# Kernel optimization log

Hardware: AMD Instinct MI355X
Metric: run time of the kernel (lower is better)

Reference implementation:

```python
import jax, jax.numpy as jnp
import numpy as np

K = 31            # kernel_size
P = K // 2        # padding
EPS = 1e-05
STRENGTH = 1.0


def _box_filter(x):
    """31x31 mean box filter with zero padding, done as two separable 1D passes.
    Exactly equals F.conv2d(x, ones(K,K)/K^2, padding=P) since the box kernel
    is separable and padding is zero-fill."""
    kh = jnp.ones((1, 1, K, 1), x.dtype) / K  # vertical pass
    kw = jnp.ones((1, 1, 1, K), x.dtype) / K  # horizontal pass
    dn = jax.lax.conv_dimension_numbers(x.shape, kh.shape, ('NCHW', 'OIHW', 'NCHW'))
    x = jax.lax.conv_general_dilated(x, kh, (1, 1), [(P, P), (0, 0)], dimension_numbers=dn)
    x = jax.lax.conv_general_dilated(x, kw, (1, 1), [(0, 0), (P, P)], dimension_numbers=dn)
    return x


def setup_inputs() -> dict:
    key = jax.random.key(0)
    # (B, 1, H, W) image in [0, 1]
    x = jax.random.uniform(key, (32, 1, 1024, 1024), dtype=jnp.float32)
    return {"x": x}


def reference(x):
    local_mean = _box_filter(x)
    local_sq_mean = _box_filter(x * x)
    local_var = local_sq_mean - local_mean * local_mean
    local_std = jnp.sqrt(jnp.maximum(local_var, EPS))  # clamp(min=eps) then sqrt
    normalized = (x - local_mean) / (local_std + EPS)
    enhanced = jax.nn.sigmoid(normalized * 0.5)
    return x * (1.0 - STRENGTH) + enhanced * STRENGTH
```

## Files before the change

### kernel.cpp

```cpp
#include <hip/hip_runtime.h>
#include <math.h>


#define KSZ   31
#define PAD   15
#define IMG_H 1024
#define IMG_W 1024
#define SH    32
#define RPP   4
#define PHASES (SH / RPP)
#define NT    256
#define LROW  66
#define LBUF  (16 * LROW)
#define EPSV  1e-5f

__global__ __launch_bounds__(NT, 4)
void lcn_fused_kernel(const float* __restrict__ x, float* __restrict__ out) {
    const int cpx = gridDim.x >> 3;
    const int bid = (blockIdx.x & 7) * cpx + (blockIdx.x >> 3);

    const int t     = threadIdx.x;
    const int chunk = bid & 31;
    const int b     = bid >> 5;
    const int y0    = chunk * SH;

    const float* img  = x   + (size_t)b * (IMG_H * IMG_W);
    float*       oimg = out + (size_t)b * (IMG_H * IMG_W);

    __shared__ float2 vbuf[RPP][LBUF];

    for (int i = t; i < RPP * LBUF; i += NT)
        (&vbuf[0][0])[i] = make_float2(0.f, 0.f);

    const int c0 = 4 * t;
    float vs0 = 0.f, vs1 = 0.f, vs2 = 0.f, vs3 = 0.f;
    float vq0 = 0.f, vq1 = 0.f, vq2 = 0.f, vq3 = 0.f;
    for (int y = y0 - PAD; y <= y0 + PAD; ++y) {
        if (y < 0) continue;
        float4 v = *(const float4*)(img + (size_t)y * IMG_W + c0);
        vs0 += v.x; vq0 += v.x * v.x;
        vs1 += v.y; vq1 += v.y * v.y;
        vs2 += v.z; vq2 += v.z * v.z;
        vs3 += v.w; vq3 += v.w * v.w;
    }

    int wp0, wp1, wp2, wp3;
    {
        const int iv = c0 + 16;
        wp0 = ((iv    ) & 15) * LROW + ((iv    ) >> 4);
        wp1 = ((iv + 1) & 15) * LROW + ((iv + 1) >> 4);
        wp2 = ((iv + 2) & 15) * LROW + ((iv + 2) >> 4);
        wp3 = ((iv + 3) & 15) * LROW + ((iv + 3) >> 4);
    }

    const int wave  = t >> 6;
    const int lane  = t & 63;
    const int cbase = lane << 4;
    const float inv = 1.0f / 961.0f;

    for (int ph = 0; ph < PHASES; ++ph) {
        const int yo = y0 + ph * RPP;

        #pragma unroll
        for (int r = 0; r < RPP; ++r) {
            vbuf[r][wp0] = make_float2(vs0, vq0);
            vbuf[r][wp1] = make_float2(vs1, vq1);
            vbuf[r][wp2] = make_float2(vs2, vq2);
            vbuf[r][wp3] = make_float2(vs3, vq3);
            const int row  = yo + r;
            const int ysub = row - PAD;
            const int yadd = row + PAD + 1;
            if (ysub >= 0) {
                float4 v = *(const float4*)(img + (size_t)ysub * IMG_W + c0);
                vs0 -= v.x; vq0 -= v.x * v.x;
                vs1 -= v.y; vq1 -= v.y * v.y;
                vs2 -= v.z; vq2 -= v.z * v.z;
                vs3 -= v.w; vq3 -= v.w * v.w;
            }
            if (yadd < IMG_H) {
                float4 v = *(const float4*)(img + (size_t)yadd * IMG_W + c0);
                vs0 += v.x; vq0 += v.x * v.x;
                vs1 += v.y; vq1 += v.y * v.y;
                vs2 += v.z; vq2 += v.z * v.z;
                vs3 += v.w; vq3 += v.w * v.w;
            }
        }
        __syncthreads();

        {
            const int row = yo + wave;
            const float2* vr = &vbuf[wave][lane];

            float hs = 0.f, hq = 0.f;
            #pragma unroll
            for (int s = 1; s <= 31; ++s) {
                const int off = (s & 15) * LROW + (s >> 4);
                float2 v = vr[off];
                hs += v.x; hq += v.y;
            }

            const float* xr = img + (size_t)row * IMG_W + cbase;
            float4 xa = ((const float4*)xr)[0];
            float4 xb = ((const float4*)xr)[1];
            float4 xc = ((const float4*)xr)[2];
            float4 xd = ((const float4*)xr)[3];
            float xs[16] = { xa.x, xa.y, xa.z, xa.w,  xb.x, xb.y, xb.z, xb.w,
                             xc.x, xc.y, xc.z, xc.w,  xd.x, xd.y, xd.z, xd.w };

            float res[16];
            #pragma unroll
            for (int j = 0; j < 16; ++j) {
                if (j > 0) {
                    float2 va = vr[((j - 1) & 15) * LROW + 2];
                    float2 vb = vr[j * LROW];
                    hs += va.x - vb.x;
                    hq += va.y - vb.y;
                }
                const float mean = hs * inv;
                const float var  = fmaf(-mean, mean, hq * inv);
                const float stdv = sqrtf(fmaxf(var, EPSV));
                const float norm = (xs[j] - mean) *
                                   __builtin_amdgcn_rcpf(stdv + EPSV);
                const float e    = __expf(-0.5f * norm);
                res[j] = __builtin_amdgcn_rcpf(1.0f + e);
            }

            float* orow = oimg + (size_t)row * IMG_W + cbase;
            ((float4*)orow)[0] = make_float4(res[0],  res[1],  res[2],  res[3]);
            ((float4*)orow)[1] = make_float4(res[4],  res[5],  res[6],  res[7]);
            ((float4*)orow)[2] = make_float4(res[8],  res[9],  res[10], res[11]);
            ((float4*)orow)[3] = make_float4(res[12], res[13], res[14], res[15]);
        }
        __syncthreads();
    }
}

extern "C" void kernel_launch(void* const* d_in, const int* in_sizes, int n_in,
                              void* d_out, int out_size, void* d_ws, size_t ws_size,
                              hipStream_t stream) {
    (void)n_in; (void)out_size; (void)d_ws; (void)ws_size;
    const float* x = (const float*)d_in[0];
    float* out = (float*)d_out;
    const int B = in_sizes[0] / (IMG_H * IMG_W);
    dim3 grid(B * (IMG_H / SH));
    lcn_fused_kernel<<<grid, NT, 0, stream>>>(x, out);
}
```

Baseline: 92.45 us.

## Give each wave its own 8-row strip and drop block-wide barriers

Each wave now owns an 8-row strip and a full 1024-column row, with 16 vertical running sums per lane in registers. It uses a private LDS buffer, so __syncthreads is replaced by s_waitcnt lgkmcnt. Loads for the next slide are issued before the horizontal pass so they overlap with compute. In exchange, every wave repeats the 31-row vertical prefix, which adds redundant global reads, and register pressure rises from the 32 accumulators.

```diff
diff --git a/kernel.cpp b/kernel.cpp
--- a/kernel.cpp
+++ b/kernel.cpp
@@ -6,9 +6,9 @@
 #define PAD   15
 #define IMG_H 1024
 #define IMG_W 1024
-#define SH    32
-#define RPP   4
-#define PHASES (SH / RPP)
+#define RPW   8
+#define WPB   4
+#define SH    (RPW * WPB)
 #define NT    256
 #define LROW  66
 #define LBUF  (16 * LROW)
@@ -19,7 +19,6 @@
     const int cpx = gridDim.x >> 3;
     const int bid = (blockIdx.x & 7) * cpx + (blockIdx.x >> 3);
 
-    const int t     = threadIdx.x;
     const int chunk = bid & 31;
     const int b     = bid >> 5;
     const int y0    = chunk * SH;
@@ -27,111 +26,152 @@
     const float* img  = x   + (size_t)b * (IMG_H * IMG_W);
     float*       oimg = out + (size_t)b * (IMG_H * IMG_W);
 
-    __shared__ float2 vbuf[RPP][LBUF];
+    __shared__ float2 vbuf[WPB][LBUF];
 
-    for (int i = t; i < RPP * LBUF; i += NT)
-        (&vbuf[0][0])[i] = make_float2(0.f, 0.f);
+    const int t    = threadIdx.x;
+    const int wave = t >> 6;
+    const int lane = t & 63;
+    float2* vb = vbuf[wave];
 
-    const int c0 = 4 * t;
-    float vs0 = 0.f, vs1 = 0.f, vs2 = 0.f, vs3 = 0.f;
-    float vq0 = 0.f, vq1 = 0.f, vq2 = 0.f, vq3 = 0.f;
-    for (int y = y0 - PAD; y <= y0 + PAD; ++y) {
-        if (y < 0) continue;
-        float4 v = *(const float4*)(img + (size_t)y * IMG_W + c0);
-        vs0 += v.x; vq0 += v.x * v.x;
-        vs1 += v.y; vq1 += v.y * v.y;
-        vs2 += v.z; vq2 += v.z * v.z;
-        vs3 += v.w; vq3 += v.w * v.w;
+    if (lane < 16) {
+        vb[lane * LROW]            = make_float2(0.f, 0.f);
+        vb[lane * LROW + LROW - 1] = make_float2(0.f, 0.f);
     }
 
-    int wp0, wp1, wp2, wp3;
-    {
-        const int iv = c0 + 16;
-        wp0 = ((iv    ) & 15) * LROW + ((iv    ) >> 4);
-        wp1 = ((iv + 1) & 15) * LROW + ((iv + 1) >> 4);
-        wp2 = ((iv + 2) & 15) * LROW + ((iv + 2) >> 4);
-        wp3 = ((iv + 3) & 15) * LROW + ((iv + 3) >> 4);
+    const int r0 = y0 + wave * RPW;
+    const int cv = 4 * lane;
+
+    float vsA[16], vqA[16];
+    #pragma unroll
+    for (int i = 0; i < 16; ++i) { vsA[i] = 0.f; vqA[i] = 0.f; }
+
+    for (int y = r0 - PAD; y <= r0 + PAD; ++y) {
+        if (y < 0 || y >= IMG_H) continue;
+        const float* rp = img + (size_t)y * IMG_W + cv;
+        #pragma unroll
+        for (int j = 0; j < 4; ++j) {
+            float4 v = *(const float4*)(rp + 256 * j);
+            vsA[4*j+0] += v.x; vqA[4*j+0] += v.x * v.x;
+            vsA[4*j+1] += v.y; vqA[4*j+1] += v.y * v.y;
+            vsA[4*j+2] += v.z; vqA[4*j+2] += v.z * v.z;
+            vsA[4*j+3] += v.w; vqA[4*j+3] += v.w * v.w;
+        }
     }
 
-    const int wave  = t >> 6;
-    const int lane  = t & 63;
-    const int cbase = lane << 4;
-    const float inv = 1.0f / 961.0f;
+    const int pb = (lane >> 2) + 1;
+    const int g0 = 4 * (lane & 3);
 
-    for (int ph = 0; ph < PHASES; ++ph) {
-        const int yo = y0 + ph * RPP;
+    const int   cbase = lane << 4;
+    const float inv   = 1.0f / 961.0f;
+
+    #pragma unroll 1
+    for (int r = 0; r < RPW; ++r) {
+        const int row = r0 + r;
 
         #pragma unroll
-        for (int r = 0; r < RPP; ++r) {
-            vbuf[r][wp0] = make_float2(vs0, vq0);
-            vbuf[r][wp1] = make_float2(vs1, vq1);
-            vbuf[r][wp2] = make_float2(vs2, vq2);
-            vbuf[r][wp3] = make_float2(vs3, vq3);
-            const int row  = yo + r;
-            const int ysub = row - PAD;
-            const int yadd = row + PAD + 1;
-            if (ysub >= 0) {
-                float4 v = *(const float4*)(img + (size_t)ysub * IMG_W + c0);
-                vs0 -= v.x; vq0 -= v.x * v.x;
-                vs1 -= v.y; vq1 -= v.y * v.y;
-                vs2 -= v.z; vq2 -= v.z * v.z;
-                vs3 -= v.w; vq3 -= v.w * v.w;
-            }
-            if (yadd < IMG_H) {
-                float4 v = *(const float4*)(img + (size_t)yadd * IMG_W + c0);
-                vs0 += v.x; vq0 += v.x * v.x;
-                vs1 += v.y; vq1 += v.y * v.y;
-                vs2 += v.z; vq2 += v.z * v.z;
-                vs3 += v.w; vq3 += v.w * v.w;
-            }
+        for (int j = 0; j < 4; ++j) {
+            vb[(g0 + 0) * LROW + pb + 16 * j] = make_float2(vsA[4*j+0], vqA[4*j+0]);
+            vb[(g0 + 1) * LROW + pb + 16 * j] = make_float2(vsA[4*j+1], vqA[4*j+1]);
+            vb[(g0 + 2) * LROW + pb + 16 * j] = make_float2(vsA[4*j+2], vqA[4*j+2]);
+            vb[(g0 + 3) * LROW + pb + 16 * j] = make_float2(vsA[4*j+3], vqA[4*j+3]);
         }
-        __syncthreads();
+        asm volatile("s_waitcnt lgkmcnt(0)" ::: "memory");
 
-        {
-            const int row = yo + wave;
-            const float2* vr = &vbuf[wave][lane];
+        const int ysub = row - PAD;
+        const int yadd = row + PAD + 1;
+        const bool do_slide = (r < RPW - 1);
+        const bool has_sub  = do_slide && (ysub >= 0);
+        const bool has_add  = do_slide && (yadd < IMG_H);
+        float4 sb0, sb1, sb2, sb3, ad0, ad1, ad2, ad3;
+        if (has_sub) {
+            const float* rp = img + (size_t)ysub * IMG_W + cv;
+            sb0 = *(const float4*)(rp      );
+            sb1 = *(const float4*)(rp + 256);
+            sb2 = *(const float4*)(rp + 512);
+            sb3 = *(const float4*)(rp + 768);
+        }
+        if (has_add) {
+            const float* rp = img + (size_t)yadd * IMG_W + cv;
+            ad0 = *(const float4*)(rp      );
+            ad1 = *(const float4*)(rp + 256);
+            ad2 = *(const float4*)(rp + 512);
+            ad3 = *(const float4*)(rp + 768);
+        }
 
-            float hs = 0.f, hq = 0.f;
+        const float2* vr = vb + lane;
+        float hs = 0.f, hq = 0.f;
+        #pragma unroll
+        for (int s = 1; s <= 31; ++s) {
+            float2 v = vr[(s & 15) * LROW + (s >> 4)];
+            hs += v.x; hq += v.y;
+        }
+
+        const float* xr   = img  + (size_t)row * IMG_W + cbase;
+        float*       orow = oimg + (size_t)row * IMG_W + cbase;
+
+        #pragma unroll
+        for (int g = 0; g < 4; ++g) {
+            float4 xv = ((const float4*)xr)[g];
+            float rz[4];
             #pragma unroll
-            for (int s = 1; s <= 31; ++s) {
-                const int off = (s & 15) * LROW + (s >> 4);
-                float2 v = vr[off];
-                hs += v.x; hq += v.y;
-            }
-
-            const float* xr = img + (size_t)row * IMG_W + cbase;
-            float4 xa = ((const float4*)xr)[0];
-            float4 xb = ((const float4*)xr)[1];
-            float4 xc = ((const float4*)xr)[2];
-            float4 xd = ((const float4*)xr)[3];
-            float xs[16] = { xa.x, xa.y, xa.z, xa.w,  xb.x, xb.y, xb.z, xb.w,
-                             xc.x, xc.y, xc.z, xc.w,  xd.x, xd.y, xd.z, xd.w };
-
-            float res[16];
-            #pragma unroll
-            for (int j = 0; j < 16; ++j) {
+            for (int j4 = 0; j4 < 4; ++j4) {
+                const int j = 4 * g + j4;
                 if (j > 0) {
                     float2 va = vr[((j - 1) & 15) * LROW + 2];
-                    float2 vb = vr[j * LROW];
-                    hs += va.x - vb.x;
-                    hq += va.y - vb.y;
+                    float2 vsu = vr[(j & 15) * LROW];
+                    hs += va.x - vsu.x;
+                    hq += va.y - vsu.y;
                 }
                 const float mean = hs * inv;
                 const float var  = fmaf(-mean, mean, hq * inv);
                 const float stdv = sqrtf(fmaxf(var, EPSV));
-                const float norm = (xs[j] - mean) *
+                const float xc   = (j4 == 0) ? xv.x : (j4 == 1) ? xv.y
+                                 : (j4 == 2) ? xv.z : xv.w;
+                const float norm = (xc - mean) *
                                    __builtin_amdgcn_rcpf(stdv + EPSV);
                 const float e    = __expf(-0.5f * norm);
-                res[j] = __builtin_amdgcn_rcpf(1.0f + e);
+                rz[j4] = __builtin_amdgcn_rcpf(1.0f + e);
             }
+            ((float4*)orow)[g] = make_float4(rz[0], rz[1], rz[2], rz[3]);
+        }
 
-            float* orow = oimg + (size_t)row * IMG_W + cbase;
-            ((float4*)orow)[0] = make_float4(res[0],  res[1],  res[2],  res[3]);
-            ((float4*)orow)[1] = make_float4(res[4],  res[5],  res[6],  res[7]);
-            ((float4*)orow)[2] = make_float4(res[8],  res[9],  res[10], res[11]);
-            ((float4*)orow)[3] = make_float4(res[12], res[13], res[14], res[15]);
+        if (has_sub) {
+            vsA[0] -= sb0.x; vqA[0] = fmaf(-sb0.x, sb0.x, vqA[0]);
+            vsA[1] -= sb0.y; vqA[1] = fmaf(-sb0.y, sb0.y, vqA[1]);
+            vsA[2] -= sb0.z; vqA[2] = fmaf(-sb0.z, sb0.z, vqA[2]);
+            vsA[3] -= sb0.w; vqA[3] = fmaf(-sb0.w, sb0.w, vqA[3]);
+            vsA[4] -= sb1.x; vqA[4] = fmaf(-sb1.x, sb1.x, vqA[4]);
+            vsA[5] -= sb1.y; vqA[5] = fmaf(-sb1.y, sb1.y, vqA[5]);
+            vsA[6] -= sb1.z; vqA[6] = fmaf(-sb1.z, sb1.z, vqA[6]);
+            vsA[7] -= sb1.w; vqA[7] = fmaf(-sb1.w, sb1.w, vqA[7]);
+            vsA[8] -= sb2.x; vqA[8] = fmaf(-sb2.x, sb2.x, vqA[8]);
+            vsA[9] -= sb2.y; vqA[9] = fmaf(-sb2.y, sb2.y, vqA[9]);
+            vsA[10]-= sb2.z; vqA[10]= fmaf(-sb2.z, sb2.z, vqA[10]);
+            vsA[11]-= sb2.w; vqA[11]= fmaf(-sb2.w, sb2.w, vqA[11]);
+            vsA[12]-= sb3.x; vqA[12]= fmaf(-sb3.x, sb3.x, vqA[12]);
+            vsA[13]-= sb3.y; vqA[13]= fmaf(-sb3.y, sb3.y, vqA[13]);
+            vsA[14]-= sb3.z; vqA[14]= fmaf(-sb3.z, sb3.z, vqA[14]);
+            vsA[15]-= sb3.w; vqA[15]= fmaf(-sb3.w, sb3.w, vqA[15]);
         }
-        __syncthreads();
+        if (has_add) {
+            vsA[0] += ad0.x; vqA[0] = fmaf(ad0.x, ad0.x, vqA[0]);
+            vsA[1] += ad0.y; vqA[1] = fmaf(ad0.y, ad0.y, vqA[1]);
+            vsA[2] += ad0.z; vqA[2] = fmaf(ad0.z, ad0.z, vqA[2]);
+            vsA[3] += ad0.w; vqA[3] = fmaf(ad0.w, ad0.w, vqA[3]);
+            vsA[4] += ad1.x; vqA[4] = fmaf(ad1.x, ad1.x, vqA[4]);
+            vsA[5] += ad1.y; vqA[5] = fmaf(ad1.y, ad1.y, vqA[5]);
+            vsA[6] += ad1.z; vqA[6] = fmaf(ad1.z, ad1.z, vqA[6]);
+            vsA[7] += ad1.w; vqA[7] = fmaf(ad1.w, ad1.w, vqA[7]);
+            vsA[8] += ad2.x; vqA[8] = fmaf(ad2.x, ad2.x, vqA[8]);
+            vsA[9] += ad2.y; vqA[9] = fmaf(ad2.y, ad2.y, vqA[9]);
+            vsA[10]+= ad2.z; vqA[10]= fmaf(ad2.z, ad2.z, vqA[10]);
+            vsA[11]+= ad2.w; vqA[11]= fmaf(ad2.w, ad2.w, vqA[11]);
+            vsA[12]+= ad3.x; vqA[12]= fmaf(ad3.x, ad3.x, vqA[12]);
+            vsA[13]+= ad3.y; vqA[13]= fmaf(ad3.y, ad3.y, vqA[13]);
+            vsA[14]+= ad3.z; vqA[14]= fmaf(ad3.z, ad3.z, vqA[14]);
+            vsA[15]+= ad3.w; vqA[15]= fmaf(ad3.w, ad3.w, vqA[15]);
+        }
+        asm volatile("s_waitcnt lgkmcnt(0)" ::: "memory");
     }
 }
 
```

New measurement: 274.8 us. 197% more time.

## Split image columns into two halves with halo columns to double block count

Applied to the files above, without the earlier changes.

Each block now handles a 512-column half of a 32-row strip, so the grid doubles and each thread carries two columns instead of four. Halo columns are kept as vertical running sums by every eighth thread, and the shared buffer is rebuilt with an 8-way interleave and padded row stride. Per phase, the vertical-update loads for all four rows and the x values are issued ahead of the shared-memory writes, and launch bounds rise to 8 blocks per CU. The cost is extra redundant halo loads and some thread divergence on the halo path.

```diff
diff --git a/kernel.cpp b/kernel.cpp
--- a/kernel.cpp
+++ b/kernel.cpp
@@ -6,131 +6,142 @@
 #define PAD   15
 #define IMG_H 1024
 #define IMG_W 1024
+#define CW    512
 #define SH    32
 #define RPP   4
-#define PHASES (SH / RPP)
 #define NT    256
-#define LROW  66
-#define LBUF  (16 * LROW)
+#define HALO  16
+#define LROW  69
+#define LBUF  (8 * LROW)
 #define EPSV  1e-5f
 
-__global__ __launch_bounds__(NT, 4)
+__global__ __launch_bounds__(NT, 8)
 void lcn_fused_kernel(const float* __restrict__ x, float* __restrict__ out) {
     const int cpx = gridDim.x >> 3;
     const int bid = (blockIdx.x & 7) * cpx + (blockIdx.x >> 3);
 
-    const int t     = threadIdx.x;
-    const int chunk = bid & 31;
-    const int b     = bid >> 5;
-    const int y0    = chunk * SH;
+    const int xc = bid & 1;
+    const int yc = (bid >> 1) & 31;
+    const int b  = bid >> 6;
+    const int y0 = yc * SH;
+    const int x0 = xc * CW;
 
     const float* img  = x   + (size_t)b * (IMG_H * IMG_W);
     float*       oimg = out + (size_t)b * (IMG_H * IMG_W);
 
     __shared__ float2 vbuf[RPP][LBUF];
 
-    for (int i = t; i < RPP * LBUF; i += NT)
-        (&vbuf[0][0])[i] = make_float2(0.f, 0.f);
+    const int t    = threadIdx.x;
+    const int wave = t >> 6;
+    const int lane = t & 63;
 
-    const int c0 = 4 * t;
-    float vs0 = 0.f, vs1 = 0.f, vs2 = 0.f, vs3 = 0.f;
-    float vq0 = 0.f, vq1 = 0.f, vq2 = 0.f, vq3 = 0.f;
-    for (int y = y0 - PAD; y <= y0 + PAD; ++y) {
-        if (y < 0) continue;
-        float4 v = *(const float4*)(img + (size_t)y * IMG_W + c0);
-        vs0 += v.x; vq0 += v.x * v.x;
-        vs1 += v.y; vq1 += v.y * v.y;
-        vs2 += v.z; vq2 += v.z * v.z;
-        vs3 += v.w; vq3 += v.w * v.w;
+    const int lci = 2 * t;
+    const int gci = x0 + lci;
+
+    const bool isH  = (t & 7) == 0;
+    const int  hidx = t >> 3;
+    const int  gchr = (hidx < 16) ? (x0 - HALO + hidx)
+                                  : (x0 + CW + (hidx - 16));
+    const bool hval = isH && (gchr >= 0) && (gchr < IMG_W);
+    const int  gch  = min(max(gchr, 0), IMG_W - 1);
+
+    const int iv0 = lci + HALO;
+    const int wp0 = ((iv0    ) & 7) * LROW + ((iv0    ) >> 3);
+    const int wp1 = ((iv0 + 1) & 7) * LROW + ((iv0 + 1) >> 3);
+    const int ivh = (hidx < 16) ? hidx : (CW + HALO + (hidx - 16));
+    const int wph = (ivh & 7) * LROW + (ivh >> 3);
+
+    float vs0 = 0.f, vq0 = 0.f, vs1 = 0.f, vq1 = 0.f, hvs = 0.f, hvq = 0.f;
+    for (int yy = y0 - PAD; yy <= y0 + PAD; ++yy) {
+        const int yyc = max(yy, 0);
+        float2 v = *(const float2*)(img + (size_t)yyc * IMG_W + gci);
+        const float m = (yy >= 0) ? 1.f : 0.f;
+        v.x *= m; v.y *= m;
+        vs0 += v.x; vq0 = fmaf(v.x, v.x, vq0);
+        vs1 += v.y; vq1 = fmaf(v.y, v.y, vq1);
+        if (isH) {
+            float h = img[(size_t)yyc * IMG_W + gch];
+            h = (hval && yy >= 0) ? h : 0.f;
+            hvs += h; hvq = fmaf(h, h, hvq);
+        }
     }
 
-    int wp0, wp1, wp2, wp3;
-    {
-        const int iv = c0 + 16;
-        wp0 = ((iv    ) & 15) * LROW + ((iv    ) >> 4);
-        wp1 = ((iv + 1) & 15) * LROW + ((iv + 1) >> 4);
-        wp2 = ((iv + 2) & 15) * LROW + ((iv + 2) >> 4);
-        wp3 = ((iv + 3) & 15) * LROW + ((iv + 3) >> 4);
-    }
-
-    const int wave  = t >> 6;
-    const int lane  = t & 63;
-    const int cbase = lane << 4;
+    const int   lc0 = lane << 3;
     const float inv = 1.0f / 961.0f;
 
-    for (int ph = 0; ph < PHASES; ++ph) {
+    for (int ph = 0; ph < SH / RPP; ++ph) {
         const int yo = y0 + ph * RPP;
+
+        float2 sb[RPP], ad[RPP];
+        #pragma unroll
+        for (int r = 0; r < RPP; ++r) {
+            const int ys  = yo - PAD + r;
+            const int ya  = yo + PAD + 1 + r;
+            const int ysc = max(ys, 0);
+            const int yac = min(ya, IMG_H - 1);
+            float2 vS = *(const float2*)(img + (size_t)ysc * IMG_W + gci);
+            float2 vA = *(const float2*)(img + (size_t)yac * IMG_W + gci);
+            const float mS = (ys >= 0)    ? 1.f : 0.f;
+            const float mA = (ya < IMG_H) ? 1.f : 0.f;
+            sb[r] = make_float2(vS.x * mS, vS.y * mS);
+            ad[r] = make_float2(vA.x * mA, vA.y * mA);
+        }
+        const int myrow = yo + wave;
+        const float* xr = img + (size_t)myrow * IMG_W + x0 + lc0;
+        const float4 xva = ((const float4*)xr)[0];
+        const float4 xvb = ((const float4*)xr)[1];
 
         #pragma unroll
         for (int r = 0; r < RPP; ++r) {
             vbuf[r][wp0] = make_float2(vs0, vq0);
             vbuf[r][wp1] = make_float2(vs1, vq1);
-            vbuf[r][wp2] = make_float2(vs2, vq2);
-            vbuf[r][wp3] = make_float2(vs3, vq3);
-            const int row  = yo + r;
-            const int ysub = row - PAD;
-            const int yadd = row + PAD + 1;
-            if (ysub >= 0) {
-                float4 v = *(const float4*)(img + (size_t)ysub * IMG_W + c0);
-                vs0 -= v.x; vq0 -= v.x * v.x;
-                vs1 -= v.y; vq1 -= v.y * v.y;
-                vs2 -= v.z; vq2 -= v.z * v.z;
-                vs3 -= v.w; vq3 -= v.w * v.w;
+            if (isH) {
+                vbuf[r][wph] = make_float2(hvs, hvq);
+                const int ys  = yo - PAD + r;
+                const int ya  = yo + PAD + 1 + r;
+                const int ysc = max(ys, 0);
+                const int yac = min(ya, IMG_H - 1);
+                float hS = img[(size_t)ysc * IMG_W + gch];
+                float hA = img[(size_t)yac * IMG_W + gch];
+                hS = (hval && ys >= 0)    ? hS : 0.f;
+                hA = (hval && ya < IMG_H) ? hA : 0.f;
+                hvs += hA - hS;
+                hvq = fmaf(hA, hA, hvq); hvq = fmaf(-hS, hS, hvq);
             }
-            if (yadd < IMG_H) {
-                float4 v = *(const float4*)(img + (size_t)yadd * IMG_W + c0);
-                vs0 += v.x; vq0 += v.x * v.x;
-                vs1 += v.y; vq1 += v.y * v.y;
-                vs2 += v.z; vq2 += v.z * v.z;
-                vs3 += v.w; vq3 += v.w * v.w;
-            }
+            vs0 += ad[r].x - sb[r].x;
+            vq0 = fmaf(ad[r].x, ad[r].x, vq0); vq0 = fmaf(-sb[r].x, sb[r].x, vq0);
+            vs1 += ad[r].y - sb[r].y;
+            vq1 = fmaf(ad[r].y, ad[r].y, vq1); vq1 = fmaf(-sb[r].y, sb[r].y, vq1);
         }
         __syncthreads();
 
-        {
-            const int row = yo + wave;
-            const float2* vr = &vbuf[wave][lane];
-
-            float hs = 0.f, hq = 0.f;
-            #pragma unroll
-            for (int s = 1; s <= 31; ++s) {
-                const int off = (s & 15) * LROW + (s >> 4);
-                float2 v = vr[off];
-                hs += v.x; hq += v.y;
+        const float2* vr = &vbuf[wave][lane];
+        float hs = 0.f, hq = 0.f;
+        #pragma unroll
+        for (int s = 1; s <= 31; ++s) {
+            float2 v = vr[(s & 7) * LROW + (s >> 3)];
+            hs += v.x; hq += v.y;
+        }
+        float res[8];
+        #pragma unroll
+        for (int j = 0; j < 8; ++j) {
+            if (j > 0) {
+                float2 va  = vr[((j + 31) & 7) * LROW + ((j + 31) >> 3)];
+                float2 vb2 = vr[(j & 7) * LROW + (j >> 3)];
+                hs += va.x - vb2.x;
+                hq += va.y - vb2.y;
             }
-
-            const float* xr = img + (size_t)row * IMG_W + cbase;
-            float4 xa = ((const float4*)xr)[0];
-            float4 xb = ((const float4*)xr)[1];
-            float4 xc = ((const float4*)xr)[2];
-            float4 xd = ((const float4*)xr)[3];
-            float xs[16] = { xa.x, xa.y, xa.z, xa.w,  xb.x, xb.y, xb.z, xb.w,
-                             xc.x, xc.y, xc.z, xc.w,  xd.x, xd.y, xd.z, xd.w };
-
-            float res[16];
-            #pragma unroll
-            for (int j = 0; j < 16; ++j) {
-                if (j > 0) {
-                    float2 va = vr[((j - 1) & 15) * LROW + 2];
-                    float2 vb = vr[j * LROW];
-                    hs += va.x - vb.x;
-                    hq += va.y - vb.y;
-                }
-                const float mean = hs * inv;
-                const float var  = fmaf(-mean, mean, hq * inv);
-                const float stdv = sqrtf(fmaxf(var, EPSV));
-                const float norm = (xs[j] - mean) *
-                                   __builtin_amdgcn_rcpf(stdv + EPSV);
-                const float e    = __expf(-0.5f * norm);
-                res[j] = __builtin_amdgcn_rcpf(1.0f + e);
-            }
-
-            float* orow = oimg + (size_t)row * IMG_W + cbase;
-            ((float4*)orow)[0] = make_float4(res[0],  res[1],  res[2],  res[3]);
-            ((float4*)orow)[1] = make_float4(res[4],  res[5],  res[6],  res[7]);
-            ((float4*)orow)[2] = make_float4(res[8],  res[9],  res[10], res[11]);
-            ((float4*)orow)[3] = make_float4(res[12], res[13], res[14], res[15]);
+            const float mean = hs * inv;
+            const float var  = fmaf(-mean, mean, hq * inv);
+            const float stdv = sqrtf(fmaxf(var, EPSV));
+            const float xcv  = (j==0)?xva.x:(j==1)?xva.y:(j==2)?xva.z:(j==3)?xva.w
+                              :(j==4)?xvb.x:(j==5)?xvb.y:(j==6)?xvb.z:xvb.w;
+            const float norm = (xcv - mean) * __builtin_amdgcn_rcpf(stdv + EPSV);
+            res[j] = __builtin_amdgcn_rcpf(1.0f + __expf(-0.5f * norm));
         }
+        float* orow = oimg + (size_t)myrow * IMG_W + x0 + lc0;
+        ((float4*)orow)[0] = make_float4(res[0], res[1], res[2], res[3]);
+        ((float4*)orow)[1] = make_float4(res[4], res[5], res[6], res[7]);
         __syncthreads();
     }
 }
@@ -142,6 +153,6 @@
     const float* x = (const float*)d_in[0];
     float* out = (float*)d_out;
     const int B = in_sizes[0] / (IMG_H * IMG_W);
-    dim3 grid(B * (IMG_H / SH));
+    dim3 grid(B * (IMG_H / SH) * (IMG_W / CW));
     lcn_fused_kernel<<<grid, NT, 0, stream>>>(x, out);
 }
```

Result: slower. 144.4 us (+56.2%).

## Prefetch next phase's rows into registers and trim LDS zero-initialisation

Applied to the files above, without the earlier changes.

Software-pipelines the global loads: the subtract/add rows for the vertical running sum and the centre x row for the next phase are loaded into registers while the current phase does its horizontal pass and output. Out-of-range rows become clamped loads multiplied by a mask instead of branches. Only the two padding columns of the shared buffer are zeroed, not the whole buffer. The aim is to hide global memory latency behind compute, at the cost of more registers per thread, which may pressure occupancy under the 4-blocks launch bound.

```diff
diff --git a/kernel.cpp b/kernel.cpp
--- a/kernel.cpp
+++ b/kernel.cpp
@@ -2,24 +2,23 @@
 #include <math.h>
 
 
-#define KSZ   31
-#define PAD   15
-#define IMG_H 1024
-#define IMG_W 1024
-#define SH    32
-#define RPP   4
+#define KSZ    31
+#define PAD    15
+#define IMG_H  1024
+#define IMG_W  1024
+#define SH     32
+#define RPP    4
 #define PHASES (SH / RPP)
-#define NT    256
-#define LROW  66
-#define LBUF  (16 * LROW)
-#define EPSV  1e-5f
+#define NT     256
+#define LROW   66
+#define LBUF   (16 * LROW)
+#define EPSV   1e-5f
 
 __global__ __launch_bounds__(NT, 4)
 void lcn_fused_kernel(const float* __restrict__ x, float* __restrict__ out) {
     const int cpx = gridDim.x >> 3;
     const int bid = (blockIdx.x & 7) * cpx + (blockIdx.x >> 3);
 
-    const int t     = threadIdx.x;
     const int chunk = bid & 31;
     const int b     = bid >> 5;
     const int y0    = chunk * SH;
@@ -29,19 +28,29 @@
 
     __shared__ float2 vbuf[RPP][LBUF];
 
-    for (int i = t; i < RPP * LBUF; i += NT)
-        (&vbuf[0][0])[i] = make_float2(0.f, 0.f);
+    const int t    = threadIdx.x;
+    const int wave = t >> 6;
+    const int lane = t & 63;
+
+    for (int i = t; i < RPP * 32; i += NT) {
+        const int r = i >> 5, k = i & 31;
+        float2* vb = vbuf[r];
+        if (k < 16) vb[k * LROW] = make_float2(0.f, 0.f);
+        else        vb[(k - 16) * LROW + (LROW - 1)] = make_float2(0.f, 0.f);
+    }
 
     const int c0 = 4 * t;
     float vs0 = 0.f, vs1 = 0.f, vs2 = 0.f, vs3 = 0.f;
     float vq0 = 0.f, vq1 = 0.f, vq2 = 0.f, vq3 = 0.f;
     for (int y = y0 - PAD; y <= y0 + PAD; ++y) {
-        if (y < 0) continue;
-        float4 v = *(const float4*)(img + (size_t)y * IMG_W + c0);
-        vs0 += v.x; vq0 += v.x * v.x;
-        vs1 += v.y; vq1 += v.y * v.y;
-        vs2 += v.z; vq2 += v.z * v.z;
-        vs3 += v.w; vq3 += v.w * v.w;
+        const int yc = max(y, 0);
+        float4 v = *(const float4*)(img + (size_t)yc * IMG_W + c0);
+        const float m = (y >= 0) ? 1.f : 0.f;
+        v.x *= m; v.y *= m; v.z *= m; v.w *= m;
+        vs0 += v.x; vq0 = fmaf(v.x, v.x, vq0);
+        vs1 += v.y; vq1 = fmaf(v.y, v.y, vq1);
+        vs2 += v.z; vq2 = fmaf(v.z, v.z, vq2);
+        vs3 += v.w; vq3 = fmaf(v.w, v.w, vq3);
     }
 
     int wp0, wp1, wp2, wp3;
@@ -53,10 +62,29 @@
         wp3 = ((iv + 3) & 15) * LROW + ((iv + 3) >> 4);
     }
 
-    const int wave  = t >> 6;
-    const int lane  = t & 63;
-    const int cbase = lane << 4;
-    const float inv = 1.0f / 961.0f;
+    const int   cbase = lane << 4;
+    const float inv   = 1.0f / 961.0f;
+
+    float4 sb[RPP], ad[RPP];
+    float4 xa, xb, xc, xd;
+    {
+        #pragma unroll
+        for (int r = 0; r < RPP; ++r) {
+            const int ys = y0 + r - PAD;
+            const int ya = y0 + r + PAD + 1;
+            const int ysc = max(ys, 0);
+            float4 vS = *(const float4*)(img + (size_t)ysc * IMG_W + c0);
+            float4 vA = *(const float4*)(img + (size_t)ya  * IMG_W + c0);
+            const float mS = (ys >= 0) ? 1.f : 0.f;
+            vS.x *= mS; vS.y *= mS; vS.z *= mS; vS.w *= mS;
+            sb[r] = vS; ad[r] = vA;
+        }
+        const float* xr = img + (size_t)(y0 + wave) * IMG_W + cbase;
+        xa = ((const float4*)xr)[0]; xb = ((const float4*)xr)[1];
+        xc = ((const float4*)xr)[2]; xd = ((const float4*)xr)[3];
+    }
+
+    __syncthreads();
 
     for (int ph = 0; ph < PHASES; ++ph) {
         const int yo = y0 + ph * RPP;
@@ -67,70 +95,75 @@
             vbuf[r][wp1] = make_float2(vs1, vq1);
             vbuf[r][wp2] = make_float2(vs2, vq2);
             vbuf[r][wp3] = make_float2(vs3, vq3);
-            const int row  = yo + r;
-            const int ysub = row - PAD;
-            const int yadd = row + PAD + 1;
-            if (ysub >= 0) {
-                float4 v = *(const float4*)(img + (size_t)ysub * IMG_W + c0);
-                vs0 -= v.x; vq0 -= v.x * v.x;
-                vs1 -= v.y; vq1 -= v.y * v.y;
-                vs2 -= v.z; vq2 -= v.z * v.z;
-                vs3 -= v.w; vq3 -= v.w * v.w;
-            }
-            if (yadd < IMG_H) {
-                float4 v = *(const float4*)(img + (size_t)yadd * IMG_W + c0);
-                vs0 += v.x; vq0 += v.x * v.x;
-                vs1 += v.y; vq1 += v.y * v.y;
-                vs2 += v.z; vq2 += v.z * v.z;
-                vs3 += v.w; vq3 += v.w * v.w;
-            }
+            vs0 += ad[r].x - sb[r].x;
+            vq0 = fmaf(ad[r].x, ad[r].x, vq0); vq0 = fmaf(-sb[r].x, sb[r].x, vq0);
+            vs1 += ad[r].y - sb[r].y;
+            vq1 = fmaf(ad[r].y, ad[r].y, vq1); vq1 = fmaf(-sb[r].y, sb[r].y, vq1);
+            vs2 += ad[r].z - sb[r].z;
+            vq2 = fmaf(ad[r].z, ad[r].z, vq2); vq2 = fmaf(-sb[r].z, sb[r].z, vq2);
+            vs3 += ad[r].w - sb[r].w;
+            vq3 = fmaf(ad[r].w, ad[r].w, vq3); vq3 = fmaf(-sb[r].w, sb[r].w, vq3);
         }
         __syncthreads();
 
+        if (ph < PHASES - 1) {
+            const int yn = yo + RPP;
+            #pragma unroll
+            for (int r = 0; r < RPP; ++r) {
+                const int ys = yn + r - PAD;
+                const int ya = yn + r + PAD + 1;
+                const int ysc = max(ys, 0);
+                const int yac = min(ya, IMG_H - 1);
+                float4 vS = *(const float4*)(img + (size_t)ysc * IMG_W + c0);
+                float4 vA = *(const float4*)(img + (size_t)yac * IMG_W + c0);
+                const float mS = (ys >= 0)    ? 1.f : 0.f;
+                const float mA = (ya < IMG_H) ? 1.f : 0.f;
+                vS.x *= mS; vS.y *= mS; vS.z *= mS; vS.w *= mS;
+                vA.x *= mA; vA.y *= mA; vA.z *= mA; vA.w *= mA;
+                sb[r] = vS; ad[r] = vA;
+            }
+        }
+        float4 nxa, nxb, nxc, nxd;
+        if (ph < PHASES - 1) {
+            const float* xr = img + (size_t)(yo + RPP + wave) * IMG_W + cbase;
+            nxa = ((const float4*)xr)[0]; nxb = ((const float4*)xr)[1];
+            nxc = ((const float4*)xr)[2]; nxd = ((const float4*)xr)[3];
+        }
+
         {
-            const int row = yo + wave;
             const float2* vr = &vbuf[wave][lane];
-
             float hs = 0.f, hq = 0.f;
             #pragma unroll
             for (int s = 1; s <= 31; ++s) {
-                const int off = (s & 15) * LROW + (s >> 4);
-                float2 v = vr[off];
+                float2 v = vr[(s & 15) * LROW + (s >> 4)];
                 hs += v.x; hq += v.y;
             }
-
-            const float* xr = img + (size_t)row * IMG_W + cbase;
-            float4 xa = ((const float4*)xr)[0];
-            float4 xb = ((const float4*)xr)[1];
-            float4 xc = ((const float4*)xr)[2];
-            float4 xd = ((const float4*)xr)[3];
             float xs[16] = { xa.x, xa.y, xa.z, xa.w,  xb.x, xb.y, xb.z, xb.w,
                              xc.x, xc.y, xc.z, xc.w,  xd.x, xd.y, xd.z, xd.w };
-
             float res[16];
             #pragma unroll
             for (int j = 0; j < 16; ++j) {
                 if (j > 0) {
-                    float2 va = vr[((j - 1) & 15) * LROW + 2];
-                    float2 vb = vr[j * LROW];
-                    hs += va.x - vb.x;
-                    hq += va.y - vb.y;
+                    float2 va  = vr[((j - 1) & 15) * LROW + 2];
+                    float2 vsu = vr[(j & 15) * LROW];
+                    hs += va.x - vsu.x;
+                    hq += va.y - vsu.y;
                 }
                 const float mean = hs * inv;
                 const float var  = fmaf(-mean, mean, hq * inv);
                 const float stdv = sqrtf(fmaxf(var, EPSV));
                 const float norm = (xs[j] - mean) *
                                    __builtin_amdgcn_rcpf(stdv + EPSV);
-                const float e    = __expf(-0.5f * norm);
-                res[j] = __builtin_amdgcn_rcpf(1.0f + e);
+                res[j] = __builtin_amdgcn_rcpf(1.0f + __expf(-0.5f * norm));
             }
-
-            float* orow = oimg + (size_t)row * IMG_W + cbase;
+            float* orow = oimg + (size_t)(yo + wave) * IMG_W + cbase;
             ((float4*)orow)[0] = make_float4(res[0],  res[1],  res[2],  res[3]);
             ((float4*)orow)[1] = make_float4(res[4],  res[5],  res[6],  res[7]);
             ((float4*)orow)[2] = make_float4(res[8],  res[9],  res[10], res[11]);
             ((float4*)orow)[3] = make_float4(res[12], res[13], res[14], res[15]);
         }
+
+        xa = nxa; xb = nxb; xc = nxc; xd = nxd;
         __syncthreads();
     }
 }
```

Result: slower. 101.1 us (+9.4%).
